# Kernel optimization log

Measured on AMD Instinct MI355X. Metric: run time of the kernel, lower is better.

Reference implementation:

```python
import jax, jax.numpy as jnp
import numpy as np

B, S, D, H = 2, 2048, 1024, 16
DK = D // H
NEG = -65504.0  # matches torch masked_fill value in source


def setup_inputs() -> dict:
    key = jax.random.key(0)
    ks = jax.random.split(key, 5)
    scale = 1.0 / np.sqrt(D)
    return {
        "x": jax.random.normal(ks[0], (B, S, D), dtype=jnp.float32),
        "W_q": jax.random.normal(ks[1], (D, D), dtype=jnp.float32) * scale,
        "W_k": jax.random.normal(ks[2], (D, D), dtype=jnp.float32) * scale,
        "W_v": jax.random.normal(ks[3], (D, D), dtype=jnp.float32) * scale,
        "W_o": jax.random.normal(ks[4], (D, D), dtype=jnp.float32) * scale,
    }


def reference(x, W_q, W_k, W_v, W_o):
    b, s, d = x.shape
    # nn.Linear(x) = x @ W.T ; split heads -> [b, h, s, dk]
    def proj(W):
        return (x @ W.T).reshape(b, s, H, DK).transpose(0, 2, 1, 3)
    q, k, v = proj(W_q), proj(W_k), proj(W_v)
    scores = jnp.einsum("bhqd,bhkd->bhqk", q, k) / jnp.sqrt(jnp.float32(DK))
    causal = jnp.tril(jnp.ones((s, s), dtype=bool))  # True where attending allowed
    scores = jnp.where(causal, scores, NEG)
    attn = jax.nn.softmax(scores, axis=-1)  # attn_pdrop=0 -> dropout is identity
    out = jnp.einsum("bhqk,bhkd->bhqd", attn, v)
    out = out.transpose(0, 2, 1, 3).reshape(b, s, d)
    return out @ W_o.T
```

## Files before the change

### kernel.cpp

```cpp
#include <hip/hip_runtime.h>
#include <hip/hip_bf16.h>

typedef __attribute__((ext_vector_type(4))) float f32x4;
typedef __attribute__((ext_vector_type(8))) short bf16x8;

#define Bn 2
#define Sn 2048
#define Dn 1024
#define Hn 16
#define DKn 64
#define Mrows (Bn * Sn)

__device__ __forceinline__ unsigned short f2bf(float f) {
  unsigned int x = __float_as_uint(f);
  x += 0x7fffu + ((x >> 16) & 1u);
  return (unsigned short)(x >> 16);
}

__device__ __forceinline__ float bf2f(unsigned short u) {
  return __uint_as_float(((unsigned int)u) << 16);
}

__device__ __forceinline__ unsigned int cvtpk(float lo, float hi) {
  unsigned int r;
  asm("v_cvt_pk_bf16_f32 %0, %1, %2" : "=v"(r) : "v"(lo), "v"(hi));
  return r;
}

__device__ __forceinline__ f32x4 mfma16(bf16x8 a, bf16x8 b, f32x4 c) {
  return __builtin_amdgcn_mfma_f32_16x16x32_bf16(a, b, c, 0, 0, 0);
}

__device__ __forceinline__ void gload_lds16(const unsigned short* g, unsigned short* l) {
  __builtin_amdgcn_global_load_lds(
      (const __attribute__((address_space(1))) void*)g,
      (__attribute__((address_space(3))) void*)l, 16, 0, 0);
}

__global__ __launch_bounds__(256)
void cvt_all(const float* __restrict__ x,  const float* __restrict__ wq,
             const float* __restrict__ wk, const float* __restrict__ wv,
             const float* __restrict__ wo,
             unsigned short* __restrict__ xb,  unsigned short* __restrict__ wqb,
             unsigned short* __restrict__ wkb, unsigned short* __restrict__ wvb,
             unsigned short* __restrict__ wob) {
  int i = (blockIdx.x * 256 + threadIdx.x) * 4;
  const float* src; unsigned short* dst; int off;
  int r = i >> 20;
  if (r < 4)       { src = x;  dst = xb;  off = i; }
  else if (r == 4) { src = wq; dst = wqb; off = i & 1048575; }
  else if (r == 5) { src = wk; dst = wkb; off = i & 1048575; }
  else if (r == 6) { src = wv; dst = wvb; off = i & 1048575; }
  else             { src = wo; dst = wob; off = i & 1048575; }
  float4 v = *(const float4*)(src + off);
  ushort4 o;
  o.x = f2bf(v.x); o.y = f2bf(v.y); o.z = f2bf(v.z); o.w = f2bf(v.w);
  *(ushort4*)(dst + off) = o;
}

template<int MODE>
__device__ __forceinline__ void gemm_body(const unsigned short* __restrict__ A,
                                          const unsigned short* __restrict__ W,
                                          unsigned short* __restrict__ Cb,
                                          float* __restrict__ Cf,
                                          unsigned short* As,
                                          unsigned short* Bs) {
  const int K = Dn, N = Dn;
  const int tid  = threadIdx.x;
  const int wid  = tid >> 6;
  const int lane = tid & 63;
  const int l15  = lane & 15;
  const int lg   = lane >> 4;
  const int row0 = blockIdx.x * 128;
  const int col0 = blockIdx.y * 128;
  const int wr = (wid >> 1) * 64;
  const int wc = (wid & 1) * 64;

  f32x4 acc[4][4] = {};

  const int lrow  = lane >> 3;
  const int sgran = (lane & 7) ^ lrow;
  const int swz   = l15 & 7;

  for (int kt = 0; kt < K; kt += 64) {
#pragma unroll
    for (int p = 0; p < 4; ++p) {
      int chunk = p * 4 + wid;
      int r = chunk * 8 + lrow;
      gload_lds16(A + (size_t)(row0 + r) * K + kt + sgran * 8, &As[chunk * 512]);
    }
#pragma unroll
    for (int p = 0; p < 4; ++p) {
      int chunk = p * 4 + wid;
      int r = chunk * 8 + lrow;
      gload_lds16(W + (size_t)(col0 + r) * K + kt + sgran * 8, &Bs[chunk * 512]);
    }
    __syncthreads();

#pragma unroll
    for (int kk = 0; kk < 2; ++kk) {
      bf16x8 af[4], bfr[4];
#pragma unroll
      for (int m = 0; m < 4; ++m)
        af[m] = *(const bf16x8*)(&As[(wr + m * 16 + l15) * 64 +
                                     (((kk * 4 + lg) ^ swz) * 8)]);
#pragma unroll
      for (int n = 0; n < 4; ++n)
        bfr[n] = *(const bf16x8*)(&Bs[(wc + n * 16 + l15) * 64 +
                                      (((kk * 4 + lg) ^ swz) * 8)]);
#pragma unroll
      for (int m = 0; m < 4; ++m)
#pragma unroll
        for (int n = 0; n < 4; ++n)
          acc[m][n] = mfma16(af[m], bfr[n], acc[m][n]);
    }
    __syncthreads();
  }

#pragma unroll
  for (int m = 0; m < 4; ++m)
#pragma unroll
    for (int n = 0; n < 4; ++n) {
      int r0 = row0 + wr + m * 16 + lg * 4;
      int c  = col0 + wc + n * 16 + l15;
      if (MODE == 2) {
        int b = r0 >> 11, s = r0 & 2047;
        int h = c >> 6,  d = c & 63;
        ushort4 pw;
        pw.x = f2bf(acc[m][n][0]); pw.y = f2bf(acc[m][n][1]);
        pw.z = f2bf(acc[m][n][2]); pw.w = f2bf(acc[m][n][3]);
        *(ushort4*)(Cb + ((((size_t)b * Hn + h) * DKn + d) << 11) + s) = pw;
      } else {
#pragma unroll
        for (int j = 0; j < 4; ++j) {
          size_t idx = (size_t)(r0 + j) * N + c;
          float v = acc[m][n][j];
          if (MODE == 3)      Cf[idx] = v;
          else if (MODE == 0) Cb[idx] = f2bf(v * 0.125f);
          else                Cb[idx] = f2bf(v);
        }
      }
    }
}

__global__ __launch_bounds__(256)
void gemm_qkv(const unsigned short* __restrict__ A,
              const unsigned short* __restrict__ W0,
              const unsigned short* __restrict__ W1,
              const unsigned short* __restrict__ W2,
              unsigned short* __restrict__ C0,
              unsigned short* __restrict__ C1,
              unsigned short* __restrict__ C2) {
  __shared__ unsigned short As[128 * 64];
  __shared__ unsigned short Bs[128 * 64];
  if (blockIdx.z == 0)      gemm_body<0>(A, W0, C0, nullptr, As, Bs);
  else if (blockIdx.z == 1) gemm_body<1>(A, W1, C1, nullptr, As, Bs);
  else                      gemm_body<2>(A, W2, C2, nullptr, As, Bs);
}

__global__ __launch_bounds__(256)
void gemm_out(const unsigned short* __restrict__ A,
              const unsigned short* __restrict__ W,
              float* __restrict__ C) {
  __shared__ unsigned short As[128 * 64];
  __shared__ unsigned short Bs[128 * 64];
  gemm_body<3>(A, W, nullptr, C, As, Bs);
}

__global__ __launch_bounds__(256)
void attn_part(const unsigned short* __restrict__ Qg,
               const unsigned short* __restrict__ Kg,
               const unsigned short* __restrict__ Vtg,
               unsigned short* __restrict__ Og,
               unsigned short* __restrict__ Pb,
               float* __restrict__ Pml) {
  const int bid = blockIdx.x;
  const int bh = bid & 31;
  const int j  = bid >> 5;
  const int bb = bh >> 4, hh = bh & 15;
  const int tid = threadIdx.x, wid = tid >> 6, lane = tid & 63;
  const int l15 = lane & 15, lg = lane >> 4;
  const int wq = wid * 32;
  const size_t baseQ = (size_t)bb * Sn * Dn + (size_t)hh * DKn;
  const size_t baseV = (size_t)bh * DKn * Sn;

  __shared__ unsigned short Ks[2][64 * 64];
  __shared__ unsigned short Vts[2][64 * 64];
  __shared__ unsigned short Ps[4][32 * 72];

  const int lrow  = lane >> 3;
  const int sgran = (lane & 7) ^ lrow;
  const int swz   = l15 & 7;

  const int g0 = 17 * j;
  int qt = 0;
  while ((qt + 1) * (qt + 2) <= g0) ++qt;
  int kt = g0 - qt * (qt + 1);

  int sqt = qt, skt = kt;
  auto stage = [&](int t, int b) {
    const int k0 = t << 6;
#pragma unroll
    for (int p = 0; p < 2; ++p) {
      int c = p * 4 + wid;
      int r = c * 8 + lrow;
      gload_lds16(Kg + baseQ + (size_t)(k0 + r) * Dn + sgran * 8, &Ks[b][c * 512]);
    }
#pragma unroll
    for (int p = 0; p < 2; ++p) {
      int c = p * 4 + wid;
      int dr = c * 8 + lrow;
      gload_lds16(Vtg + baseV + (size_t)dr * Sn + k0 + sgran * 8, &Vts[b][c * 512]);
    }
  };
  auto advs = [&]() { ++skt; if (skt == 2 * sqt + 2) { skt = 0; ++sqt; } };

  stage(skt, 0); advs();
  __syncthreads();

  bf16x8 qf[2][2];
  auto loadQ = [&](int qtile) {
    const int q0 = qtile * 128;
#pragma unroll
    for (int qm = 0; qm < 2; ++qm)
#pragma unroll
      for (int kd = 0; kd < 2; ++kd)
        qf[qm][kd] = *(const bf16x8*)(Qg + baseQ +
                     (size_t)(q0 + wq + qm * 16 + l15) * Dn + kd * 32 + lg * 8);
  };
  loadQ(qt);

  f32x4 oacc[2][4] = {};
  float mrun[2] = {-1e30f, -1e30f};
  float lrun[2] = {0.f, 0.f};
  int pstart = kt;

  for (int i = 0; i < 17; ++i) {
    const int cur = i & 1;
    if (i < 16) { stage(skt, cur ^ 1); advs(); }
    const int k0 = kt << 6;
    const int q0 = qt * 128;

    if (k0 <= q0 + wq + 31) {
      f32x4 sf[2][4] = {};
      __builtin_amdgcn_s_setprio(1);
#pragma unroll
      for (int kn = 0; kn < 4; ++kn)
#pragma unroll
        for (int kd = 0; kd < 2; ++kd) {
          bf16x8 kf = *(const bf16x8*)(&Ks[cur][(kn * 16 + l15) * 64 +
                                              (((kd * 4 + lg) ^ swz) * 8)]);
          sf[0][kn] = mfma16(kf, qf[0][kd], sf[0][kn]);
          sf[1][kn] = mfma16(kf, qf[1][kd], sf[1][kn]);
        }
      __builtin_amdgcn_s_setprio(0);

      if (k0 + 63 > q0 + wq) {
#pragma unroll
        for (int qm = 0; qm < 2; ++qm) {
          int qq = q0 + wq + qm * 16 + l15;
#pragma unroll
          for (int kn = 0; kn < 4; ++kn)
#pragma unroll
            for (int jj = 0; jj < 4; ++jj) {
              int key = k0 + kn * 16 + lg * 4 + jj;
              if (key > qq) sf[qm][kn][jj] = -1e30f;
            }
        }
      }

#pragma unroll
      for (int qm = 0; qm < 2; ++qm) {
        float t = sf[qm][0][0];
#pragma unroll
        for (int kn = 0; kn < 4; ++kn)
#pragma unroll
          for (int jj = 0; jj < 4; ++jj) t = fmaxf(t, sf[qm][kn][jj]);
        t = fmaxf(t, __shfl_xor(t, 16));
        t = fmaxf(t, __shfl_xor(t, 32));
        if (__any(t > mrun[qm] + 8.0f)) {
          float mnew = fmaxf(mrun[qm], t);
          float corr = __expf(mrun[qm] - mnew);
          mrun[qm] = mnew;
          lrun[qm] *= corr;
#pragma unroll
          for (int dn = 0; dn < 4; ++dn) oacc[qm][dn] *= corr;
        }
        const float m = mrun[qm];
        float rs = 0.f;
#pragma unroll
        for (int kn = 0; kn < 4; ++kn) {
#pragma unroll
          for (int jj = 0; jj < 4; ++jj) {
            float p = __expf(sf[qm][kn][jj] - m);
            sf[qm][kn][jj] = p;
            rs += p;
          }
          uint2 pw;
          pw.x = cvtpk(sf[qm][kn][0], sf[qm][kn][1]);
          pw.y = cvtpk(sf[qm][kn][2], sf[qm][kn][3]);
          *(uint2*)(&Ps[wid][(qm * 16 + l15) * 72 + kn * 16 + lg * 4]) = pw;
        }
        rs += __shfl_xor(rs, 16);
        rs += __shfl_xor(rs, 32);
        lrun[qm] += rs;
      }

      __builtin_amdgcn_s_setprio(1);
#pragma unroll
      for (int kk = 0; kk < 2; ++kk) {
        bf16x8 pf[2];
#pragma unroll
        for (int qm = 0; qm < 2; ++qm)
          pf[qm] = *(const bf16x8*)(&Ps[wid][(qm * 16 + l15) * 72 + kk * 32 + lg * 8]);
#pragma unroll
        for (int dn = 0; dn < 4; ++dn) {
          bf16x8 vf = *(const bf16x8*)(&Vts[cur][(dn * 16 + l15) * 64 +
                                               (((kk * 4 + lg) ^ swz) * 8)]);
#pragma unroll
          for (int qm = 0; qm < 2; ++qm)
            oacc[qm][dn] = mfma16(vf, pf[qm], oacc[qm][dn]);
        }
      }
      __builtin_amdgcn_s_setprio(0);
    }

    const bool segend = (kt == 2 * qt + 1);
    if (segend || i == 16) {
      if (pstart == 0 && segend) {
#pragma unroll
        for (int qm = 0; qm < 2; ++qm) {
          float rinv = 1.0f / lrun[qm];
          int row = q0 + wq + qm * 16 + l15;
#pragma unroll
          for (int dn = 0; dn < 4; ++dn) {
            ushort4 ow;
            ow.x = f2bf(oacc[qm][dn][0] * rinv);
            ow.y = f2bf(oacc[qm][dn][1] * rinv);
            ow.z = f2bf(oacc[qm][dn][2] * rinv);
            ow.w = f2bf(oacc[qm][dn][3] * rinv);
            *(ushort4*)(Og + baseQ + (size_t)row * Dn + dn * 16 + lg * 4) = ow;
          }
        }
      } else {
        const int seg_s = qt * (qt + 1);
        const int ord = pstart ? ((seg_s + pstart) / 17 - seg_s / 17) : 0;
        const size_t slot = (size_t)((bh * 16 + qt) * 3 + ord);
#pragma unroll
        for (int qm = 0; qm < 2; ++qm) {
          int rl = wq + qm * 16 + l15;
#pragma unroll
          for (int dn = 0; dn < 4; ++dn) {
            ushort4 ow;
            ow.x = f2bf(oacc[qm][dn][0]);
            ow.y = f2bf(oacc[qm][dn][1]);
            ow.z = f2bf(oacc[qm][dn][2]);
            ow.w = f2bf(oacc[qm][dn][3]);
            *(ushort4*)(Pb + slot * 8192 + (size_t)rl * 64 + dn * 16 + lg * 4) = ow;
          }
          if (lg == 0) {
            Pml[slot * 256 + rl] = mrun[qm];
            Pml[slot * 256 + 128 + rl] = lrun[qm];
          }
        }
      }
      if (i < 16) {
        ++qt; kt = 0; pstart = 0;
        loadQ(qt);
#pragma unroll
        for (int qm = 0; qm < 2; ++qm) {
          mrun[qm] = -1e30f; lrun[qm] = 0.f;
#pragma unroll
          for (int dn = 0; dn < 4; ++dn) oacc[qm][dn] = f32x4{0.f, 0.f, 0.f, 0.f};
        }
      }
    } else {
      ++kt;
    }
    __syncthreads();
  }
}

__global__ __launch_bounds__(256)
void attn_combine(const unsigned short* __restrict__ Pb,
                  const float* __restrict__ Pml,
                  unsigned short* __restrict__ Og) {
  const int b = blockIdx.x;
  const int bh = b >> 4, qt = b & 15;
  const int seg_s = qt * (qt + 1);
  const int seg_e = seg_s + 2 * qt + 2;
  const int c0 = (seg_s / 17 + 1) * 17;
  if (c0 >= seg_e) return;
  const int np = (c0 + 17 < seg_e) ? 3 : 2;
  const int bb = bh >> 4, hh = bh & 15;
  const size_t baseQ = (size_t)bb * Sn * Dn + (size_t)hh * DKn;
  const int q0 = qt * 128;
  const int slot0 = b * 3;
  const int r = threadIdx.x >> 1;
  const int c32 = (threadIdx.x & 1) * 32;

  float m0 = Pml[(size_t)slot0 * 256 + r];
  float l0 = Pml[(size_t)slot0 * 256 + 128 + r];
  float m1 = Pml[(size_t)(slot0 + 1) * 256 + r];
  float l1 = Pml[(size_t)(slot0 + 1) * 256 + 128 + r];
  float m2 = -1e30f, l2 = 0.f;
  if (np == 3) {
    m2 = Pml[(size_t)(slot0 + 2) * 256 + r];
    l2 = Pml[(size_t)(slot0 + 2) * 256 + 128 + r];
  }
  float M = fmaxf(fmaxf(m0, m1), m2);
  float w0 = __expf(m0 - M), w1 = __expf(m1 - M);
  float w2 = (np == 3) ? __expf(m2 - M) : 0.f;
  float L = l0 * w0 + l1 * w1 + l2 * w2;

  float acc[32];
#pragma unroll
  for (int k = 0; k < 32; ++k) acc[k] = 0.f;

  auto accum = [&](int p, float w) {
    const unsigned short* src = Pb + (size_t)(slot0 + p) * 8192 + (size_t)r * 64 + c32;
#pragma unroll
    for (int k4 = 0; k4 < 8; ++k4) {
      ushort4 v = *(const ushort4*)(src + k4 * 4);
      acc[k4 * 4 + 0] += w * bf2f(v.x);
      acc[k4 * 4 + 1] += w * bf2f(v.y);
      acc[k4 * 4 + 2] += w * bf2f(v.z);
      acc[k4 * 4 + 3] += w * bf2f(v.w);
    }
  };
  accum(0, w0);
  accum(1, w1);
  if (np == 3) accum(2, w2);

  float rinv = 1.0f / L;
#pragma unroll
  for (int k4 = 0; k4 < 8; ++k4) {
    ushort4 o;
    o.x = f2bf(acc[k4 * 4 + 0] * rinv);
    o.y = f2bf(acc[k4 * 4 + 1] * rinv);
    o.z = f2bf(acc[k4 * 4 + 2] * rinv);
    o.w = f2bf(acc[k4 * 4 + 3] * rinv);
    *(ushort4*)(Og + baseQ + (size_t)(q0 + r) * Dn + c32 + k4 * 4) = o;
  }
}

extern "C" void kernel_launch(void* const* d_in, const int* in_sizes, int n_in,
                              void* d_out, int out_size, void* d_ws, size_t ws_size,
                              hipStream_t stream) {
  const float* x  = (const float*)d_in[0];
  const float* Wq = (const float*)d_in[1];
  const float* Wk = (const float*)d_in[2];
  const float* Wv = (const float*)d_in[3];
  const float* Wo = (const float*)d_in[4];
  float* out = (float*)d_out;

  char* ws = (char*)d_ws;
  size_t off = 0;
  unsigned short* xb  = (unsigned short*)(ws + off); off += (size_t)Mrows * Dn * 2;
  unsigned short* wqb = (unsigned short*)(ws + off); off += (size_t)Dn * Dn * 2;
  unsigned short* wkb = (unsigned short*)(ws + off); off += (size_t)Dn * Dn * 2;
  unsigned short* wvb = (unsigned short*)(ws + off); off += (size_t)Dn * Dn * 2;
  unsigned short* wob = (unsigned short*)(ws + off); off += (size_t)Dn * Dn * 2;
  unsigned short* Qb  = (unsigned short*)(ws + off); off += (size_t)Mrows * Dn * 2;
  unsigned short* Kb  = (unsigned short*)(ws + off); off += (size_t)Mrows * Dn * 2;
  unsigned short* Vtb = (unsigned short*)(ws + off); off += (size_t)Mrows * Dn * 2;
  unsigned short* Ob  = (unsigned short*)(ws + off); off += (size_t)Mrows * Dn * 2;
  unsigned short* Pb  = (unsigned short*)(ws + off); off += (size_t)512 * 3 * 8192 * 2;
  float*          Pml = (float*)(ws + off);          off += (size_t)512 * 3 * 256 * 4;

  cvt_all<<<8192, 256, 0, stream>>>(x, Wq, Wk, Wv, Wo, xb, wqb, wkb, wvb, wob);
  gemm_qkv<<<dim3(Mrows / 128, Dn / 128, 3), 256, 0, stream>>>(xb, wqb, wkb, wvb, Qb, Kb, Vtb);
  attn_part<<<512, 256, 0, stream>>>(Qb, Kb, Vtb, Ob, Pb, Pml);
  attn_combine<<<512, 256, 0, stream>>>(Pb, Pml, Ob);
  gemm_out<<<dim3(Mrows / 128, Dn / 128), 256, 0, stream>>>(Ob, wob, out);
}
```

Measured before the change: 126.5 us.

## Triple-buffer GEMM K-loop, rebalance attention work across 768 blocks, vectorize reductions

The GEMM body now uses a K-tile of 32 with a three-stage LDS ring. Loads are issued two tiles ahead and gated by explicit vmcnt waits and a single barrier per iteration, with MFMA priority raised, so global-load latency can overlap with compute. The attention partial kernel now splits the causal tile stream into 768 chunks of roughly 11 tiles instead of 512 chunks of 17, which adds parallelism. The combine kernel and the slot layout change to handle up to four partials per query tile, and the softmax max/sum reductions are done as vector ops. It also adds occupancy hints via launch bounds of 3 blocks per CU, at the cost of more partial writes and merges.

```diff
diff --git a/kernel.cpp b/kernel.cpp
--- a/kernel.cpp
+++ b/kernel.cpp
@@ -29,6 +29,13 @@
 
 __device__ __forceinline__ f32x4 mfma16(bf16x8 a, bf16x8 b, f32x4 c) {
   return __builtin_amdgcn_mfma_f32_16x16x32_bf16(a, b, c, 0, 0, 0);
+}
+
+__device__ __forceinline__ f32x4 max4(f32x4 a, f32x4 b) {
+  f32x4 r;
+  r[0] = fmaxf(a[0], b[0]); r[1] = fmaxf(a[1], b[1]);
+  r[2] = fmaxf(a[2], b[2]); r[3] = fmaxf(a[3], b[3]);
+  return r;
 }
 
 __device__ __forceinline__ void gload_lds16(const unsigned short* g, unsigned short* l) {
@@ -78,43 +85,62 @@
 
   f32x4 acc[4][4] = {};
 
-  const int lrow  = lane >> 3;
-  const int sgran = (lane & 7) ^ lrow;
-  const int swz   = l15 & 7;
-
-  for (int kt = 0; kt < K; kt += 64) {
-#pragma unroll
-    for (int p = 0; p < 4; ++p) {
-      int chunk = p * 4 + wid;
-      int r = chunk * 8 + lrow;
-      gload_lds16(A + (size_t)(row0 + r) * K + kt + sgran * 8, &As[chunk * 512]);
-    }
-#pragma unroll
-    for (int p = 0; p < 4; ++p) {
-      int chunk = p * 4 + wid;
-      int r = chunk * 8 + lrow;
-      gload_lds16(W + (size_t)(col0 + r) * K + kt + sgran * 8, &Bs[chunk * 512]);
-    }
-    __syncthreads();
-
-#pragma unroll
-    for (int kk = 0; kk < 2; ++kk) {
-      bf16x8 af[4], bfr[4];
-#pragma unroll
-      for (int m = 0; m < 4; ++m)
-        af[m] = *(const bf16x8*)(&As[(wr + m * 16 + l15) * 64 +
-                                     (((kk * 4 + lg) ^ swz) * 8)]);
+  const int lrow2 = lane >> 2;
+  const int gs    = (lane & 3) ^ ((lane >> 3) & 3);
+  const int swzr  = (l15 >> 1) & 3;
+
+  auto stage = [&](int kt, int b) {
+#pragma unroll
+    for (int q = 0; q < 2; ++q) {
+      int chunk = wid * 2 + q;
+      int r = chunk * 16 + lrow2;
+      gload_lds16(A + (size_t)(row0 + r) * K + kt + gs * 8,
+                  &As[b * 4096 + chunk * 512]);
+    }
+#pragma unroll
+    for (int q = 0; q < 2; ++q) {
+      int chunk = wid * 2 + q;
+      int r = chunk * 16 + lrow2;
+      gload_lds16(W + (size_t)(col0 + r) * K + kt + gs * 8,
+                  &Bs[b * 4096 + chunk * 512]);
+    }
+  };
+
+  auto compute = [&](int b) {
+    bf16x8 af[4], bfr[4];
+#pragma unroll
+    for (int m = 0; m < 4; ++m)
+      af[m] = *(const bf16x8*)(&As[b * 4096 + (wr + m * 16 + l15) * 32 +
+                                   ((lg ^ swzr) * 8)]);
+#pragma unroll
+    for (int n = 0; n < 4; ++n)
+      bfr[n] = *(const bf16x8*)(&Bs[b * 4096 + (wc + n * 16 + l15) * 32 +
+                                    ((lg ^ swzr) * 8)]);
+    __builtin_amdgcn_s_setprio(1);
+#pragma unroll
+    for (int m = 0; m < 4; ++m)
 #pragma unroll
       for (int n = 0; n < 4; ++n)
-        bfr[n] = *(const bf16x8*)(&Bs[(wc + n * 16 + l15) * 64 +
-                                      (((kk * 4 + lg) ^ swz) * 8)]);
-#pragma unroll
-      for (int m = 0; m < 4; ++m)
-#pragma unroll
-        for (int n = 0; n < 4; ++n)
-          acc[m][n] = mfma16(af[m], bfr[n], acc[m][n]);
-    }
-    __syncthreads();
+        acc[m][n] = mfma16(af[m], bfr[n], acc[m][n]);
+    __builtin_amdgcn_s_setprio(0);
+  };
+
+  stage(0, 0);
+  stage(32, 1);
+  int cb = 0;
+#pragma unroll 1
+  for (int t = 0; t < 32; ++t) {
+    if (t < 31) asm volatile("s_waitcnt vmcnt(4)" ::: "memory");
+    else        asm volatile("s_waitcnt vmcnt(0)" ::: "memory");
+    __builtin_amdgcn_sched_barrier(0);
+    __builtin_amdgcn_s_barrier();
+    __builtin_amdgcn_sched_barrier(0);
+    if (t <= 29) {
+      int sb = cb + 2; if (sb >= 3) sb -= 3;
+      stage((t + 2) * 32, sb);
+    }
+    compute(cb);
+    ++cb; if (cb == 3) cb = 0;
   }
 
 #pragma unroll
@@ -143,7 +169,7 @@
     }
 }
 
-__global__ __launch_bounds__(256)
+__global__ __launch_bounds__(256, 3)
 void gemm_qkv(const unsigned short* __restrict__ A,
               const unsigned short* __restrict__ W0,
               const unsigned short* __restrict__ W1,
@@ -151,23 +177,23 @@
               unsigned short* __restrict__ C0,
               unsigned short* __restrict__ C1,
               unsigned short* __restrict__ C2) {
-  __shared__ unsigned short As[128 * 64];
-  __shared__ unsigned short Bs[128 * 64];
+  __shared__ unsigned short As[3 * 128 * 32];
+  __shared__ unsigned short Bs[3 * 128 * 32];
   if (blockIdx.z == 0)      gemm_body<0>(A, W0, C0, nullptr, As, Bs);
   else if (blockIdx.z == 1) gemm_body<1>(A, W1, C1, nullptr, As, Bs);
   else                      gemm_body<2>(A, W2, C2, nullptr, As, Bs);
 }
 
-__global__ __launch_bounds__(256)
+__global__ __launch_bounds__(256, 3)
 void gemm_out(const unsigned short* __restrict__ A,
               const unsigned short* __restrict__ W,
               float* __restrict__ C) {
-  __shared__ unsigned short As[128 * 64];
-  __shared__ unsigned short Bs[128 * 64];
+  __shared__ unsigned short As[3 * 128 * 32];
+  __shared__ unsigned short Bs[3 * 128 * 32];
   gemm_body<3>(A, W, nullptr, C, As, Bs);
 }
 
-__global__ __launch_bounds__(256)
+__global__ __launch_bounds__(256, 3)
 void attn_part(const unsigned short* __restrict__ Qg,
                const unsigned short* __restrict__ Kg,
                const unsigned short* __restrict__ Vtg,
@@ -192,10 +218,12 @@
   const int sgran = (lane & 7) ^ lrow;
   const int swz   = l15 & 7;
 
-  const int g0 = 17 * j;
+  const int bstart = (34 * j) / 3;
+  const int nt = (34 * (j + 1)) / 3 - bstart;
+
   int qt = 0;
-  while ((qt + 1) * (qt + 2) <= g0) ++qt;
-  int kt = g0 - qt * (qt + 1);
+  while ((qt + 1) * (qt + 2) <= bstart) ++qt;
+  int kt = bstart - qt * (qt + 1);
 
   int sqt = qt, skt = kt;
   auto stage = [&](int t, int b) {
@@ -235,9 +263,9 @@
   float lrun[2] = {0.f, 0.f};
   int pstart = kt;
 
-  for (int i = 0; i < 17; ++i) {
+  for (int i = 0; i < nt; ++i) {
     const int cur = i & 1;
-    if (i < 16) { stage(skt, cur ^ 1); advs(); }
+    if (i < nt - 1) { stage(skt, cur ^ 1); advs(); }
     const int k0 = kt << 6;
     const int q0 = qt * 128;
 
@@ -271,11 +299,8 @@
 
 #pragma unroll
       for (int qm = 0; qm < 2; ++qm) {
-        float t = sf[qm][0][0];
-#pragma unroll
-        for (int kn = 0; kn < 4; ++kn)
-#pragma unroll
-          for (int jj = 0; jj < 4; ++jj) t = fmaxf(t, sf[qm][kn][jj]);
+        f32x4 mm = max4(max4(sf[qm][0], sf[qm][1]), max4(sf[qm][2], sf[qm][3]));
+        float t = fmaxf(fmaxf(mm[0], mm[1]), fmaxf(mm[2], mm[3]));
         t = fmaxf(t, __shfl_xor(t, 16));
         t = fmaxf(t, __shfl_xor(t, 32));
         if (__any(t > mrun[qm] + 8.0f)) {
@@ -287,20 +312,18 @@
           for (int dn = 0; dn < 4; ++dn) oacc[qm][dn] *= corr;
         }
         const float m = mrun[qm];
-        float rs = 0.f;
 #pragma unroll
         for (int kn = 0; kn < 4; ++kn) {
 #pragma unroll
-          for (int jj = 0; jj < 4; ++jj) {
-            float p = __expf(sf[qm][kn][jj] - m);
-            sf[qm][kn][jj] = p;
-            rs += p;
-          }
+          for (int jj = 0; jj < 4; ++jj)
+            sf[qm][kn][jj] = __expf(sf[qm][kn][jj] - m);
           uint2 pw;
           pw.x = cvtpk(sf[qm][kn][0], sf[qm][kn][1]);
           pw.y = cvtpk(sf[qm][kn][2], sf[qm][kn][3]);
           *(uint2*)(&Ps[wid][(qm * 16 + l15) * 72 + kn * 16 + lg * 4]) = pw;
         }
+        f32x4 sv = (sf[qm][0] + sf[qm][1]) + (sf[qm][2] + sf[qm][3]);
+        float rs = (sv[0] + sv[1]) + (sv[2] + sv[3]);
         rs += __shfl_xor(rs, 16);
         rs += __shfl_xor(rs, 32);
         lrun[qm] += rs;
@@ -326,7 +349,7 @@
     }
 
     const bool segend = (kt == 2 * qt + 1);
-    if (segend || i == 16) {
+    if (segend || i == nt - 1) {
       if (pstart == 0 && segend) {
 #pragma unroll
         for (int qm = 0; qm < 2; ++qm) {
@@ -343,9 +366,7 @@
           }
         }
       } else {
-        const int seg_s = qt * (qt + 1);
-        const int ord = pstart ? ((seg_s + pstart) / 17 - seg_s / 17) : 0;
-        const size_t slot = (size_t)((bh * 16 + qt) * 3 + ord);
+        const size_t slot = (size_t)bh * 40 + (pstart == 0 ? qt : 16 + j);
 #pragma unroll
         for (int qm = 0; qm < 2; ++qm) {
           int rl = wq + qm * 16 + l15;
@@ -364,7 +385,7 @@
           }
         }
       }
-      if (i < 16) {
+      if (i < nt - 1) {
         ++qt; kt = 0; pstart = 0;
         loadQ(qt);
 #pragma unroll
@@ -387,38 +408,41 @@
                   unsigned short* __restrict__ Og) {
   const int b = blockIdx.x;
   const int bh = b >> 4, qt = b & 15;
-  const int seg_s = qt * (qt + 1);
-  const int seg_e = seg_s + 2 * qt + 2;
-  const int c0 = (seg_s / 17 + 1) * 17;
-  if (c0 >= seg_e) return;
-  const int np = (c0 + 17 < seg_e) ? 3 : 2;
+  const int s = qt * (qt + 1);
+  const int e = s + 2 * qt + 2;
+  const int js = (3 * s + 2) / 34;
+  const int je = (3 * (e - 1) + 2) / 34;
+  const int np = je - js + 1;
+  if (np == 1) return;
   const int bb = bh >> 4, hh = bh & 15;
   const size_t baseQ = (size_t)bb * Sn * Dn + (size_t)hh * DKn;
   const int q0 = qt * 128;
-  const int slot0 = b * 3;
   const int r = threadIdx.x >> 1;
   const int c32 = (threadIdx.x & 1) * 32;
 
-  float m0 = Pml[(size_t)slot0 * 256 + r];
-  float l0 = Pml[(size_t)slot0 * 256 + 128 + r];
-  float m1 = Pml[(size_t)(slot0 + 1) * 256 + r];
-  float l1 = Pml[(size_t)(slot0 + 1) * 256 + 128 + r];
-  float m2 = -1e30f, l2 = 0.f;
-  if (np == 3) {
-    m2 = Pml[(size_t)(slot0 + 2) * 256 + r];
-    l2 = Pml[(size_t)(slot0 + 2) * 256 + 128 + r];
-  }
-  float M = fmaxf(fmaxf(m0, m1), m2);
+  const size_t s0 = (size_t)bh * 40 + qt;
+  const size_t s1 = (size_t)bh * 40 + 16 + js + 1;
+  const size_t s2 = (size_t)bh * 40 + 16 + js + 2;
+  const size_t s3 = (size_t)bh * 40 + 16 + js + 3;
+
+  float m0 = Pml[s0 * 256 + r],      l0 = Pml[s0 * 256 + 128 + r];
+  float m1 = Pml[s1 * 256 + r],      l1 = Pml[s1 * 256 + 128 + r];
+  float m2 = -1e30f, l2 = 0.f, m3 = -1e30f, l3 = 0.f;
+  if (np > 2) { m2 = Pml[s2 * 256 + r]; l2 = Pml[s2 * 256 + 128 + r]; }
+  if (np > 3) { m3 = Pml[s3 * 256 + r]; l3 = Pml[s3 * 256 + 128 + r]; }
+
+  float M = fmaxf(fmaxf(m0, m1), fmaxf(m2, m3));
   float w0 = __expf(m0 - M), w1 = __expf(m1 - M);
-  float w2 = (np == 3) ? __expf(m2 - M) : 0.f;
-  float L = l0 * w0 + l1 * w1 + l2 * w2;
+  float w2 = (np > 2) ? __expf(m2 - M) : 0.f;
+  float w3 = (np > 3) ? __expf(m3 - M) : 0.f;
+  float L = l0 * w0 + l1 * w1 + l2 * w2 + l3 * w3;
 
   float acc[32];
 #pragma unroll
   for (int k = 0; k < 32; ++k) acc[k] = 0.f;
 
-  auto accum = [&](int p, float w) {
-    const unsigned short* src = Pb + (size_t)(slot0 + p) * 8192 + (size_t)r * 64 + c32;
+  auto accum = [&](size_t slot, float w) {
+    const unsigned short* src = Pb + slot * 8192 + (size_t)r * 64 + c32;
 #pragma unroll
     for (int k4 = 0; k4 < 8; ++k4) {
       ushort4 v = *(const ushort4*)(src + k4 * 4);
@@ -428,9 +452,10 @@
       acc[k4 * 4 + 3] += w * bf2f(v.w);
     }
   };
-  accum(0, w0);
-  accum(1, w1);
-  if (np == 3) accum(2, w2);
+  accum(s0, w0);
+  accum(s1, w1);
+  if (np > 2) accum(s2, w2);
+  if (np > 3) accum(s3, w3);
 
   float rinv = 1.0f / L;
 #pragma unroll
@@ -465,12 +490,12 @@
   unsigned short* Kb  = (unsigned short*)(ws + off); off += (size_t)Mrows * Dn * 2;
   unsigned short* Vtb = (unsigned short*)(ws + off); off += (size_t)Mrows * Dn * 2;
   unsigned short* Ob  = (unsigned short*)(ws + off); off += (size_t)Mrows * Dn * 2;
-  unsigned short* Pb  = (unsigned short*)(ws + off); off += (size_t)512 * 3 * 8192 * 2;
-  float*          Pml = (float*)(ws + off);          off += (size_t)512 * 3 * 256 * 4;
+  unsigned short* Pb  = (unsigned short*)(ws + off); off += (size_t)1280 * 8192 * 2;
+  float*          Pml = (float*)(ws + off);          off += (size_t)1280 * 256 * 4;
 
   cvt_all<<<8192, 256, 0, stream>>>(x, Wq, Wk, Wv, Wo, xb, wqb, wkb, wvb, wob);
   gemm_qkv<<<dim3(Mrows / 128, Dn / 128, 3), 256, 0, stream>>>(xb, wqb, wkb, wvb, Qb, Kb, Vtb);
-  attn_part<<<512, 256, 0, stream>>>(Qb, Kb, Vtb, Ob, Pb, Pml);
+  attn_part<<<768, 256, 0, stream>>>(Qb, Kb, Vtb, Ob, Pb, Pml);
   attn_combine<<<512, 256, 0, stream>>>(Pb, Pml, Ob);
   gemm_out<<<dim3(Mrows / 128, Dn / 128), 256, 0, stream>>>(Ob, wob, out);
 }
```

Result: faster. 112.2 us (-11.3%).
